# Performance work log

Measured on AMD Instinct MI355X. Metric: run time of the kernel, lower is better.

## Reference

```python
import jax, jax.numpy as jnp
import numpy as np

N = 64
DX = np.pi / N
# torch.fft.fftfreq(N+1, d) == np.fft.fftfreq(N+1) / d ; d varies per env so keep base freqs
BASE_FREQ = (2.0 * np.pi * np.fft.fftfreq(N + 1)).astype(np.float32)  # [65]
DOMAIN = np.array([0.75, 1.0, 0.75, 1.0, 0.75, 1.0, 0.75, 1.0], dtype=np.float32)


def _poisson_solve(w, dx_b):
    # w: [B,N,N] vorticity (already negated), dx_b: [B]
    w_pad = jnp.pad(w, ((0, 0), (0, 1), (0, 1)), mode='wrap')          # circular pad (0,1,0,1) -> [B,65,65]
    wf = jnp.fft.fft2(w_pad / (N ** 2))
    f = BASE_FREQ[None, :] / dx_b[:, None]                             # [B,65] per-env wavenumbers
    k2 = f[:, :, None] ** 2 + f[:, None, :] ** 2                       # [B,65,65] (meshgrid 'ij': kxx^2+kyy^2)
    uf = -wf / (1e-12 + k2)
    uf = uf.at[:, 0, 0].set(0.0)
    return jnp.fft.ifft2((N ** 2) * uf).real[:, :N, :N]                # [B,N,N]


def reference(t, y0, env, params):
    x = y0[:, 0]                                                       # [B,N,N]
    env = env.astype(jnp.int32)
    mu = params[env, 0][:, None, None]                                 # [B,1,1]
    fdx = (jnp.asarray(DOMAIN)[env] * DX)[:, None, None]               # [B,1,1]

    psi = _poisson_solve(-x, fdx[:, 0, 0])

    dxp = lambda a: jnp.roll(a, -1, axis=2) - jnp.roll(a, 1, axis=2)   # derive_x
    dyp = lambda a: jnp.roll(a, -1, axis=1) - jnp.roll(a, 1, axis=1)   # derive_y
    inv4 = 1.0 / (4.0 * fdx ** 2)

    J1 = (dyp(psi) * dxp(x) - dxp(psi) * dyp(x)) * inv4
    J2 = (jnp.roll(x, -1, axis=2) * dyp(jnp.roll(psi, -1, axis=2))
          - jnp.roll(x, 1, axis=2) * dyp(jnp.roll(psi, 1, axis=2))
          - jnp.roll(x, -1, axis=1) * dxp(jnp.roll(psi, -1, axis=1))
          + jnp.roll(x, 1, axis=1) * dxp(jnp.roll(psi, 1, axis=1))) * inv4
    J3 = (jnp.roll(x, (-1, -1), axis=(1, 2)) * (jnp.roll(psi, -1, axis=1) - jnp.roll(psi, -1, axis=2))
          - jnp.roll(x, (1, 1), axis=(1, 2)) * (jnp.roll(psi, 1, axis=2) - jnp.roll(psi, 1, axis=1))
          - jnp.roll(x, (-1, 1), axis=(1, 2)) * (jnp.roll(psi, -1, axis=1) - jnp.roll(psi, 1, axis=2))
          + jnp.roll(x, (1, -1), axis=(1, 2)) * (jnp.roll(psi, -1, axis=2) - jnp.roll(psi, 1, axis=1))) * inv4

    # circular-pad conv2d with kernel [[0,1,0],[1,-4,1],[1,1,0]] == cross-correlation stencil below
    lap = (jnp.roll(x, 1, axis=1) + jnp.roll(x, -1, axis=1)
           + jnp.roll(x, 1, axis=2) + jnp.roll(x, -1, axis=2)
           + jnp.roll(x, (-1, 1), axis=(1, 2)) - 4.0 * x) / (fdx ** 2)

    dudt = -(J1 + J2 + J3) / 3.0 + mu * lap
    return dudt[:, None]                                               # [B,1,N,N]


def setup_inputs() -> dict:
    key = jax.random.key(0)
    k1, k2 = jax.random.split(key)
    B, n_env = 2048, 8
    y0 = jax.random.normal(k1, (B, 1, N, N), dtype=jnp.float32)
    env = jax.random.randint(k2, (B,), 0, n_env, dtype=jnp.int64)
    params = jnp.concatenate([jnp.full((n_env, 1), 0.005, jnp.float32),
                              jnp.full((n_env, 1), 1.0, jnp.float32)], axis=1)
    t = jnp.zeros((1,), dtype=jnp.float32)
    return {"t": t, "y0": y0, "env": env, "params": params}
```

## Files before the change

### kernel.cpp

```cpp
#include <hip/hip_runtime.h>
#include <math.h>

#define P65 65
#define PLANE_U16 5248
#define SIDE_OFF  5120
#define PSI_U16   8320

__device__ __align__(16) ushort gAfrag[18*512];
__device__ float  g_MpPad[65*68];
__device__ float  g64tab[65];

__device__ __constant__ float c_DOMAIN[8] = {0.75f,1.0f,0.75f,1.0f,0.75f,1.0f,0.75f,1.0f};

__device__ inline ushort f2bf(float f) {
  unsigned u = __float_as_uint(f);
  return (ushort)((u + 0x7FFFu + ((u >> 16) & 1u)) >> 16);
}
__device__ inline float bf2f(ushort h) { return __uint_as_float(((unsigned)h) << 16); }

__device__ inline void barrier_lds() {
  asm volatile("s_waitcnt lgkmcnt(0)" ::: "memory");
  __builtin_amdgcn_sched_barrier(0);
  __builtin_amdgcn_s_barrier();
  __builtin_amdgcn_sched_barrier(0);
}

__device__ inline float Gvalf(int r, int i) {
  int m = (r <= 32) ? r : (r - 32);
  int prod = (m * (i % 65)) % 65;
  float ang = 6.2831853071795864769f * (float)prod / 65.0f;
  return (r <= 32) ? cosf(ang) : sinf(ang);
}
__device__ inline float Gfoldf(int r, int i) {
  float v = Gvalf(r, i);
  if (i == 0) v += Gvalf(r, 64);
  return v;
}

__global__ void init_tables() {
  int tid = blockIdx.x*blockDim.x + threadIdx.x;
  int nth = gridDim.x*blockDim.x;
  for (int idx = tid; idx < 18*512; idx += nth) {
    int blk = idx >> 9, rem = idx & 511;
    int lane = rem >> 3, e = rem & 7;
    int i16 = lane & 15, kg = lane >> 4;
    float v = 0.f;
    if (blk < 10) {
      int mt = blk >> 1, kt = blk & 1;
      int r = 16*mt + i16;
      int i = 32*kt + 8*kg + e;
      if (r < 65 && i < 64) v = Gfoldf(r, i);
    } else {
      int b2 = blk - 10;
      int mt = b2 >> 1, kt = b2 & 1;
      int j  = 16*mt + i16;
      int k1 = 32*kt + 8*kg + e;
      if (j < 64 && k1 < 64) v = Gvalf(k1, j);
    }
    gAfrag[idx] = f2bf(v);
  }
  for (int idx = tid; idx < 65*68; idx += nth) {
    int k2 = idx/68, k1 = idx%68;
    float v = 0.f;
    if (k1 <= 64 && (k1 | k2)) {
      float n1 = (k1==0)?(1.0f/65.0f):(2.0f/65.0f);
      float n2 = (k2==0)?(1.0f/65.0f):(2.0f/65.0f);
      int m1 = (k1<=32)?k1:(k1-32), m2 = (k2<=32)?k2:(k2-32);
      float b1 = 6.2831853071795864769f*(float)m1/65.0f;
      float b2 = 6.2831853071795864769f*(float)m2/65.0f;
      v = (n1*n2)/(b1*b1 + b2*b2);
    }
    g_MpPad[idx] = v;
  }
  for (int idx = tid; idx < 65; idx += nth)
    g64tab[idx] = (idx < 64) ? Gvalf(64, idx) : 0.f;
}

typedef __attribute__((ext_vector_type(8))) short bf16x8;
typedef __attribute__((ext_vector_type(4))) float f32x4;

template<int JT, int TBLOFF>
__device__ inline void prefetchA(bf16x8 (&pre)[2][2], int wvu, int lane, int NTL) {
  #pragma unroll
  for (int tb = 0; tb < 2; ++tb) {
    int tile = wvu + 8*tb;
    int tl = (tile < NTL) ? tile : 0;
    int jt = tl % JT;
    #pragma unroll
    for (int kt = 0; kt < 2; ++kt)
      pre[tb][kt] = *(const bf16x8*)(gAfrag + (TBLOFF + jt*2 + kt)*512 + lane*8);
  }
}

template<int IT, int JT, int TBLOFF, bool SCALE, bool RK, bool PSI>
__device__ inline void stage(const bf16x8 (&pre)[2][2],
                             const ushort* __restrict__ Lin,
                             ushort* __restrict__ Lout,
                             float* __restrict__ psiout,
                             int wvu, int lane)
{
  const int lg = lane >> 4, li = lane & 15;
  constexpr int NTL = IT*JT;
  constexpr int TPW = (NTL + 7) >> 3;
  #pragma unroll
  for (int tb = 0; tb < TPW; ++tb) {
    const int tile = wvu + 8*tb;
    if (tile >= NTL) continue;
    const int it = tile / JT, jt = tile - it*JT;
    f32x4 acc = {0.f, 0.f, 0.f, 0.f};
    #pragma unroll
    for (int kt = 0; kt < 2; ++kt) {
      bf16x8 af = (tb < 2) ? pre[tb][kt]
                           : *(const bf16x8*)(gAfrag + (TBLOFF + jt*2 + kt)*512 + lane*8);
      bf16x8 df = *(const bf16x8*)(Lin + (it*2 + kt)*512 + lane*8);
      acc = __builtin_amdgcn_mfma_f32_16x16x32_bf16(df, af, acc, 0, 0, 0);
    }
    const int f     = 16*jt + li;
    const int dbase = 16*it + 4*lg;
    const bool dEdge = (IT == 5) && (it == IT-1);
    const bool fEdge = (JT == 5) && (jt == JT-1);

    float v[4];
    #pragma unroll
    for (int r = 0; r < 4; ++r) v[r] = acc[r];

    if (SCALE) {
      const float* mp = g_MpPad + (fEdge ? 64 : f)*68 + (dEdge ? 64 : dbase);
      if (dEdge) v[0] *= mp[0];
      else {
        f32x4 m4 = *(const f32x4*)mp;
        #pragma unroll
        for (int r = 0; r < 4; ++r) v[r] *= m4[r];
      }
    }
    if (RK) {
      float gv = g64tab[f];
      uint2 sc = *(const uint2*)(Lin + SIDE_OFF + dbase);
      v[0] = fmaf(bf2f((ushort)(sc.x      )), gv, v[0]);
      v[1] = fmaf(bf2f((ushort)(sc.x >> 16)), gv, v[1]);
      v[2] = fmaf(bf2f((ushort)(sc.y      )), gv, v[2]);
      v[3] = fmaf(bf2f((ushort)(sc.y >> 16)), gv, v[3]);
    }

    if (PSI) {
      #pragma unroll
      for (int r = 0; r < 4; ++r) psiout[f*65 + dbase + r] = v[r];
    } else if (dEdge) {
      if (lg == 0 && (!fEdge || li == 0))
        Lout[SIDE_OFF + f] = f2bf(v[0]);
    } else {
      if (!fEdge || li == 0) {
        int wb = (2*jt + (it>>1))*512 + ((2*it + (lg>>1))&3)*128 + li*8 + 4*(lg&1);
        uint2 pk;
        pk.x = ((unsigned)f2bf(v[1]) << 16) | (unsigned)f2bf(v[0]);
        pk.y = ((unsigned)f2bf(v[3]) << 16) | (unsigned)f2bf(v[2]);
        *(uint2*)(Lout + wb) = pk;
      }
    }
  }
}

__device__ inline float shflx(float v, int srclane) { return __shfl(v, srclane, 64); }

__global__ void __launch_bounds__(512) pde_main(const float* __restrict__ y0,
                                                const int*   __restrict__ env,
                                                const float* __restrict__ params,
                                                float*       __restrict__ out)
{
  __shared__ __align__(16) ushort Lsh[PLANE_U16 + PSI_U16];
  ushort* PB   = Lsh;
  ushort* PA   = Lsh + PLANE_U16;
  float*  Ppsi = (float*)(Lsh + PLANE_U16);

  const int b    = blockIdx.x;
  const int t    = threadIdx.x;
  const int lane = t & 63;
  const int wvu  = __builtin_amdgcn_readfirstlane(t >> 6);

  const int   e       = env[b];
  const float mu      = params[2*e];
  const float fdx     = c_DOMAIN[e] * (float)(3.14159265358979323846/64.0);
  const float inv_dx2 = 1.0f/(fdx*fdx);

  const float* xb = y0 + (size_t)b*4096;

  const int j0 = wvu*8, jm0 = (j0+63)&63, jp8 = (j0+8)&63;
  float xbm = xb[jm0*64 + lane];
  float xbp = xb[jp8*64 + lane];

  float xr[8];
  bf16x8 hv;
  #pragma unroll
  for (int k=0;k<8;++k) {
    float v = xb[(8*wvu + k)*64 + lane];
    xr[k] = v;
    hv[k] = (short)f2bf(v);
  }
  {
    int wb = ((lane>>4)*2 + (wvu>>2))*512 + ((wvu&3)*16 + (lane&15))*8;
    *(bf16x8*)(PA + wb) = hv;
  }
  bf16x8 p1[2][2];  prefetchA<5,0>(p1, wvu, lane, 20);
  barrier_lds();

  stage<4,5, 0,false,false,false>(p1, PA, PB, nullptr, wvu, lane);
  bf16x8 p2[2][2];  prefetchA<5,0>(p2, wvu, lane, 25);
  barrier_lds();

  stage<5,5, 0,true ,false,false>(p2, PB, PA, nullptr, wvu, lane);
  bf16x8 p3[2][2];  prefetchA<4,10>(p3, wvu, lane, 20);
  barrier_lds();

  stage<5,4,10,false,true ,false>(p3, PA, PB, nullptr, wvu, lane);
  bf16x8 p4[2][2];  prefetchA<4,10>(p4, wvu, lane, 16);
  barrier_lds();

  stage<4,4,10,false,true ,true >(p4, PB, nullptr, Ppsi, wvu, lane);
  barrier_lds();

  {
    const int c = lane, cm = (c+63)&63, cp = (c+1)&63;
    const int cB = c*65, cmB = cm*65, cpB = cp*65;
    float* op = out + (size_t)b*4096;

    float xm_c = xbm,   xm_m = shflx(xm_c, cm), xm_p = shflx(xm_c, cp);
    float xc_c = xr[0], xc_m = shflx(xc_c, cm), xc_p = shflx(xc_c, cp);
    float pm_m = Ppsi[cmB+jm0], pm_c = Ppsi[cB+jm0], pm_p = Ppsi[cpB+jm0];
    float pc_m = Ppsi[cmB+j0 ], pc_c = Ppsi[cB+j0 ], pc_p = Ppsi[cpB+j0 ];

    #pragma unroll
    for (int m=0;m<8;++m) {
      int j = j0 + m, jp = (j+1)&63;
      float xn_c = (m < 7) ? xr[m+1] : xbp;
      float xn_m = shflx(xn_c, cm), xn_p = shflx(xn_c, cp);
      float pn_m = Ppsi[cmB+jp], pn_c = Ppsi[cB+jp], pn_p = Ppsi[cpB+jp];

      float J1 = (pn_c - pm_c)*(xc_p - xc_m) - (pc_p - pc_m)*(xn_c - xm_c);
      float J2 = xc_p*(pn_p - pm_p) - xc_m*(pn_m - pm_m)
               - xn_c*(pn_p - pn_m) + xm_c*(pm_p - pm_m);
      float J3 = xn_p*(pn_c - pc_p) - xm_m*(pc_m - pm_c)
               - xn_m*(pn_c - pc_m) + xm_p*(pc_p - pm_c);
      float lap = (xm_c + xn_c + xc_m + xc_p + xn_m - 4.0f*xc_c) * inv_dx2;

      op[j*64 + c] = -(J1 + J2 + J3)*(0.25f/3.0f) + mu*lap;

      xm_m=xc_m; xm_c=xc_c; xm_p=xc_p;  pm_m=pc_m; pm_c=pc_c; pm_p=pc_p;
      xc_m=xn_m; xc_c=xn_c; xc_p=xn_p;  pc_m=pn_m; pc_c=pn_c; pc_p=pn_p;
    }
  }
}

extern "C" void kernel_launch(void* const* d_in, const int* in_sizes, int n_in,
                              void* d_out, int out_size, void* d_ws, size_t ws_size,
                              hipStream_t stream) {
  const float* y0     = (const float*)d_in[1];
  const int*   env    = (const int*)  d_in[2];
  const float* params = (const float*)d_in[3];
  float*       out    = (float*)d_out;
  int B = in_sizes[1] / 4096;

  init_tables<<<64, 256, 0, stream>>>();
  pde_main<<<B, 512, 0, stream>>>(y0, env, params, out);
}
```

Measured before the change: 34.97 us.

## Process one batch element per wavefront instead of per 512-thread block

Each wavefront now handles one whole 64x64 plane, running every spectral-transform MFMA tile itself, so block-wide barriers become wave-local LDS fences. Seven waves share a block, each with its own pair of LDS buffers. The psi field is kept in LDS as bf16 rather than fp32 so it fits in the wave's buffers. The aim is to remove s_barrier synchronisation and raise independent work per CU, at the cost of serial per-wave latency, extra global reloads of x in the stencil phase, and lower precision on psi.

```diff
diff --git a/kernel.cpp b/kernel.cpp
--- a/kernel.cpp
+++ b/kernel.cpp
@@ -4,7 +4,7 @@
 #define P65 65
 #define PLANE_U16 5248
 #define SIDE_OFF  5120
-#define PSI_U16   8320
+#define NWAVE 7
 
 __device__ __align__(16) ushort gAfrag[18*512];
 __device__ float  g_MpPad[65*68];
@@ -18,10 +18,8 @@
 }
 __device__ inline float bf2f(ushort h) { return __uint_as_float(((unsigned)h) << 16); }
 
-__device__ inline void barrier_lds() {
+__device__ inline void wavefence() {
   asm volatile("s_waitcnt lgkmcnt(0)" ::: "memory");
-  __builtin_amdgcn_sched_barrier(0);
-  __builtin_amdgcn_s_barrier();
   __builtin_amdgcn_sched_barrier(0);
 }
 
@@ -79,39 +77,21 @@
 typedef __attribute__((ext_vector_type(8))) short bf16x8;
 typedef __attribute__((ext_vector_type(4))) float f32x4;
 
-template<int JT, int TBLOFF>
-__device__ inline void prefetchA(bf16x8 (&pre)[2][2], int wvu, int lane, int NTL) {
-  #pragma unroll
-  for (int tb = 0; tb < 2; ++tb) {
-    int tile = wvu + 8*tb;
-    int tl = (tile < NTL) ? tile : 0;
-    int jt = tl % JT;
-    #pragma unroll
-    for (int kt = 0; kt < 2; ++kt)
-      pre[tb][kt] = *(const bf16x8*)(gAfrag + (TBLOFF + jt*2 + kt)*512 + lane*8);
-  }
-}
-
-template<int IT, int JT, int TBLOFF, bool SCALE, bool RK, bool PSI>
-__device__ inline void stage(const bf16x8 (&pre)[2][2],
-                             const ushort* __restrict__ Lin,
-                             ushort* __restrict__ Lout,
-                             float* __restrict__ psiout,
-                             int wvu, int lane)
+template<int IT, int JT, int TBLOFF, bool SCALE, bool RK, bool PSIB>
+__device__ inline void stage1w(const ushort* __restrict__ Lin,
+                               ushort* __restrict__ Lout,
+                               ushort* __restrict__ psib,
+                               int lane)
 {
   const int lg = lane >> 4, li = lane & 15;
   constexpr int NTL = IT*JT;
-  constexpr int TPW = (NTL + 7) >> 3;
-  #pragma unroll
-  for (int tb = 0; tb < TPW; ++tb) {
-    const int tile = wvu + 8*tb;
-    if (tile >= NTL) continue;
+  #pragma unroll 4
+  for (int tile = 0; tile < NTL; ++tile) {
     const int it = tile / JT, jt = tile - it*JT;
     f32x4 acc = {0.f, 0.f, 0.f, 0.f};
     #pragma unroll
     for (int kt = 0; kt < 2; ++kt) {
-      bf16x8 af = (tb < 2) ? pre[tb][kt]
-                           : *(const bf16x8*)(gAfrag + (TBLOFF + jt*2 + kt)*512 + lane*8);
+      bf16x8 af = *(const bf16x8*)(gAfrag + (TBLOFF + jt*2 + kt)*512 + lane*8);
       bf16x8 df = *(const bf16x8*)(Lin + (it*2 + kt)*512 + lane*8);
       acc = __builtin_amdgcn_mfma_f32_16x16x32_bf16(df, af, acc, 0, 0, 0);
     }
@@ -142,9 +122,9 @@
       v[3] = fmaf(bf2f((ushort)(sc.y >> 16)), gv, v[3]);
     }
 
-    if (PSI) {
+    if (PSIB) {
       #pragma unroll
-      for (int r = 0; r < 4; ++r) psiout[f*65 + dbase + r] = v[r];
+      for (int r = 0; r < 4; ++r) psib[f*65 + dbase + r] = f2bf(v[r]);
     } else if (dEdge) {
       if (lg == 0 && (!fEdge || li == 0))
         Lout[SIDE_OFF + f] = f2bf(v[0]);
@@ -162,20 +142,24 @@
 
 __device__ inline float shflx(float v, int srclane) { return __shfl(v, srclane, 64); }
 
-__global__ void __launch_bounds__(512) pde_main(const float* __restrict__ y0,
+__global__ void __launch_bounds__(448) pde_main(const float* __restrict__ y0,
                                                 const int*   __restrict__ env,
                                                 const float* __restrict__ params,
-                                                float*       __restrict__ out)
+                                                float*       __restrict__ out,
+                                                int B)
 {
-  __shared__ __align__(16) ushort Lsh[PLANE_U16 + PSI_U16];
-  ushort* PB   = Lsh;
-  ushort* PA   = Lsh + PLANE_U16;
-  float*  Ppsi = (float*)(Lsh + PLANE_U16);
-
-  const int b    = blockIdx.x;
+  __shared__ __align__(16) ushort Lsh[NWAVE*2*PLANE_U16];
+
   const int t    = threadIdx.x;
   const int lane = t & 63;
   const int wvu  = __builtin_amdgcn_readfirstlane(t >> 6);
+
+  const int b = blockIdx.x*NWAVE + wvu;
+  if (b >= B) return;
+
+  ushort* PA   = Lsh + wvu*2*PLANE_U16;
+  ushort* PB   = PA + PLANE_U16;
+  ushort* psib = PA;
 
   const int   e       = env[b];
   const float mu      = params[2*e];
@@ -184,68 +168,68 @@
 
   const float* xb = y0 + (size_t)b*4096;
 
-  const int j0 = wvu*8, jm0 = (j0+63)&63, jp8 = (j0+8)&63;
-  float xbm = xb[jm0*64 + lane];
-  float xbp = xb[jp8*64 + lane];
-
-  float xr[8];
-  bf16x8 hv;
   #pragma unroll
-  for (int k=0;k<8;++k) {
-    float v = xb[(8*wvu + k)*64 + lane];
-    xr[k] = v;
-    hv[k] = (short)f2bf(v);
-  }
-  {
-    int wb = ((lane>>4)*2 + (wvu>>2))*512 + ((wvu&3)*16 + (lane&15))*8;
+  for (int g = 0; g < 8; ++g) {
+    bf16x8 hv;
+    #pragma unroll
+    for (int k = 0; k < 8; ++k)
+      hv[k] = (short)f2bf(xb[(8*g + k)*64 + lane]);
+    int wb = ((lane>>4)*2 + (g>>2))*512 + (16*(g&3) + (lane&15))*8;
     *(bf16x8*)(PA + wb) = hv;
   }
-  bf16x8 p1[2][2];  prefetchA<5,0>(p1, wvu, lane, 20);
-  barrier_lds();
-
-  stage<4,5, 0,false,false,false>(p1, PA, PB, nullptr, wvu, lane);
-  bf16x8 p2[2][2];  prefetchA<5,0>(p2, wvu, lane, 25);
-  barrier_lds();
-
-  stage<5,5, 0,true ,false,false>(p2, PB, PA, nullptr, wvu, lane);
-  bf16x8 p3[2][2];  prefetchA<4,10>(p3, wvu, lane, 20);
-  barrier_lds();
-
-  stage<5,4,10,false,true ,false>(p3, PA, PB, nullptr, wvu, lane);
-  bf16x8 p4[2][2];  prefetchA<4,10>(p4, wvu, lane, 16);
-  barrier_lds();
-
-  stage<4,4,10,false,true ,true >(p4, PB, nullptr, Ppsi, wvu, lane);
-  barrier_lds();
+  wavefence();
+
+  stage1w<4,5, 0,false,false,false>(PA, PB, nullptr, lane);
+  wavefence();
+  stage1w<5,5, 0,true ,false,false>(PB, PA, nullptr, lane);
+  wavefence();
+  stage1w<5,4,10,false,true ,false>(PA, PB, nullptr, lane);
+  wavefence();
+  stage1w<4,4,10,false,true ,true >(PB, nullptr, psib, lane);
+  wavefence();
 
   {
     const int c = lane, cm = (c+63)&63, cp = (c+1)&63;
-    const int cB = c*65, cmB = cm*65, cpB = cp*65;
     float* op = out + (size_t)b*4096;
 
-    float xm_c = xbm,   xm_m = shflx(xm_c, cm), xm_p = shflx(xm_c, cp);
-    float xc_c = xr[0], xc_m = shflx(xc_c, cm), xc_p = shflx(xc_c, cp);
-    float pm_m = Ppsi[cmB+jm0], pm_c = Ppsi[cB+jm0], pm_p = Ppsi[cpB+jm0];
-    float pc_m = Ppsi[cmB+j0 ], pc_c = Ppsi[cB+j0 ], pc_p = Ppsi[cpB+j0 ];
-
-    #pragma unroll
-    for (int m=0;m<8;++m) {
-      int j = j0 + m, jp = (j+1)&63;
-      float xn_c = (m < 7) ? xr[m+1] : xbp;
-      float xn_m = shflx(xn_c, cm), xn_p = shflx(xn_c, cp);
-      float pn_m = Ppsi[cmB+jp], pn_c = Ppsi[cB+jp], pn_p = Ppsi[cpB+jp];
-
-      float J1 = (pn_c - pm_c)*(xc_p - xc_m) - (pc_p - pc_m)*(xn_c - xm_c);
-      float J2 = xc_p*(pn_p - pm_p) - xc_m*(pn_m - pm_m)
-               - xn_c*(pn_p - pn_m) + xm_c*(pm_p - pm_m);
-      float J3 = xn_p*(pn_c - pc_p) - xm_m*(pc_m - pm_c)
-               - xn_m*(pn_c - pc_m) + xm_p*(pc_p - pm_c);
-      float lap = (xm_c + xn_c + xc_m + xc_p + xn_m - 4.0f*xc_c) * inv_dx2;
-
-      op[j*64 + c] = -(J1 + J2 + J3)*(0.25f/3.0f) + mu*lap;
-
-      xm_m=xc_m; xm_c=xc_c; xm_p=xc_p;  pm_m=pc_m; pm_c=pc_c; pm_p=pc_p;
-      xc_m=xn_m; xc_c=xn_c; xc_p=xn_p;  pc_m=pn_m; pc_c=pn_c; pc_p=pn_p;
+    float xm_c = xb[63*64 + c];
+    float xc_c = xb[ 0*64 + c];
+    float xm_m = shflx(xm_c, cm), xm_p = shflx(xm_c, cp);
+    float xc_m = shflx(xc_c, cm), xc_p = shflx(xc_c, cp);
+    float pm_m = bf2f(psib[cm*65+63]), pm_c = bf2f(psib[c*65+63]), pm_p = bf2f(psib[cp*65+63]);
+    float pc_m = bf2f(psib[cm*65+ 0]), pc_c = bf2f(psib[c*65+ 0]), pc_p = bf2f(psib[cp*65+ 0]);
+
+    for (int jb = 0; jb < 8; ++jb) {
+      const int j0b = jb*8;
+      float xq[8];
+      ushort qm[8], qc[8], qp[8];
+      #pragma unroll
+      for (int k = 0; k < 8; ++k) {
+        int jp = (j0b + k + 1) & 63;
+        xq[k] = xb[jp*64 + c];
+        qm[k] = psib[cm*65 + jp];
+        qc[k] = psib[c *65 + jp];
+        qp[k] = psib[cp*65 + jp];
+      }
+      #pragma unroll
+      for (int k = 0; k < 8; ++k) {
+        int j = j0b + k;
+        float xn_c = xq[k];
+        float xn_m = shflx(xn_c, cm), xn_p = shflx(xn_c, cp);
+        float pn_m = bf2f(qm[k]), pn_c = bf2f(qc[k]), pn_p = bf2f(qp[k]);
+
+        float J1 = (pn_c - pm_c)*(xc_p - xc_m) - (pc_p - pc_m)*(xn_c - xm_c);
+        float J2 = xc_p*(pn_p - pm_p) - xc_m*(pn_m - pm_m)
+                 - xn_c*(pn_p - pn_m) + xm_c*(pm_p - pm_m);
+        float J3 = xn_p*(pn_c - pc_p) - xm_m*(pc_m - pm_c)
+                 - xn_m*(pn_c - pc_m) + xm_p*(pc_p - pm_c);
+        float lap = (xm_c + xn_c + xc_m + xc_p + xn_m - 4.0f*xc_c) * inv_dx2;
+
+        op[j*64 + c] = -(J1 + J2 + J3)*(0.25f/3.0f) + mu*lap;
+
+        xm_m=xc_m; xm_c=xc_c; xm_p=xc_p;  pm_m=pc_m; pm_c=pc_c; pm_p=pc_p;
+        xc_m=xn_m; xc_c=xn_c; xc_p=xn_p;  pc_m=pn_m; pc_c=pn_c; pc_p=pn_p;
+      }
     }
   }
 }
@@ -258,7 +242,8 @@
   const float* params = (const float*)d_in[3];
   float*       out    = (float*)d_out;
   int B = in_sizes[1] / 4096;
+  int nb = (B + NWAVE - 1) / NWAVE;
 
   init_tables<<<64, 256, 0, stream>>>();
-  pde_main<<<B, 512, 0, stream>>>(y0, env, params, out);
-}
+  pde_main<<<nb, 448, 0, stream>>>(y0, env, params, out, B);
+}
```

Measured after the change: 64.53 us. +84.5%, slower.
